# Performance work log

Hardware: AMD Instinct MI355X
Metric: run time of the kernel (lower is better)

Reference implementation:

```python
import jax, jax.numpy as jnp
import numpy as np

HID = 128      # hidden_features
NF = 32        # noise_features
NPL = NF // 4  # noise features per layer
RES = 512      # noise grid resolution
N = 262144     # number of query points


def leaky_relu(x):
    return jax.nn.leaky_relu(x, negative_slope=0.01)


def sample_bilinear(image, coords):
    """image: [M, H, W]; coords: [..., M, 2] -> [..., M]"""
    M, Hn, Wn = image.shape
    x = coords[..., 0] - 0.5
    y = coords[..., 1] - 0.5
    x0f = jnp.floor(x)
    y0f = jnp.floor(y)
    xw = x - x0f
    yw = y - y0f
    x0 = x0f.astype(jnp.int32) % Wn
    x1 = (x0f.astype(jnp.int32) + 1) % Wn
    y0 = y0f.astype(jnp.int32) % Hn
    y1 = (y0f.astype(jnp.int32) + 1) % Hn
    f = jnp.arange(M)  # broadcasts against [..., M] index arrays
    i00 = image[f, y0, x0]
    i01 = image[f, y0, x1]
    i10 = image[f, y1, x0]
    i11 = image[f, y1, x1]
    i0 = i00 + (i01 - i00) * xw
    i1 = i10 + (i11 - i10) * xw
    return i0 + (i1 - i0) * yw


def setup_inputs() -> dict:
    key = jax.random.key(0)
    ks = jax.random.split(key, 12)
    noise = jax.random.normal(ks[0], (NF, RES, RES), dtype=jnp.float32)
    coords = jax.random.normal(ks[1], (N, 2), dtype=jnp.float32)
    # NoiseTransforms param: randn * 0.05 * 2**i per feature
    scale = 0.05 * (2.0 ** np.arange(NF)).astype(np.float32)
    transformations = jax.random.normal(ks[2], (NF, 2, 2), dtype=jnp.float32) * scale[:, None, None]
    input_vec = jnp.ones((HID,), dtype=jnp.float32)
    s_lin = 1.0 / np.sqrt(HID)
    s_noise = 1.0 / np.sqrt(NPL)
    lw = jax.random.uniform(ks[3], (4, HID, HID), jnp.float32, -s_lin, s_lin)
    lb = jax.random.uniform(ks[4], (4, HID), jnp.float32, -s_lin, s_lin)
    lnw = jax.random.uniform(ks[5], (4, HID, NPL), jnp.float32, -s_noise, s_noise)
    tw1 = jax.random.uniform(ks[6], (HID, HID), jnp.float32, -s_lin, s_lin)
    tb1 = jax.random.uniform(ks[7], (HID,), jnp.float32, -s_lin, s_lin)
    tw2 = jax.random.uniform(ks[8], (1, HID), jnp.float32, -s_lin, s_lin)
    tb2 = jax.random.uniform(ks[9], (1,), jnp.float32, -s_lin, s_lin)
    return {"noise": noise, "coords": coords, "transformations": transformations,
            "input_vec": input_vec, "lw": lw, "lb": lb, "lnw": lnw,
            "tw1": tw1, "tb1": tb1, "tw2": tw2, "tb2": tb2}


def reference(noise, coords, transformations, input_vec, lw, lb, lnw, tw1, tb1, tw2, tb2):
    # noise coords: [..., NF, 2]
    noise_coords = jnp.einsum('...n,Mmn->...Mm', coords, transformations)
    noise_values = sample_bilinear(noise, noise_coords)  # [..., NF]
    x = input_vec  # [HID], broadcasts up through layer adds
    for i in range(4):
        nv = noise_values[..., i * NPL:(i + 1) * NPL]
        x = leaky_relu(jnp.einsum('...h,oh->...o', x, lw[i]) + lb[i]
                       + jnp.einsum('...n,on->...o', nv, lnw[i]))
    h = leaky_relu(jnp.einsum('...h,oh->...o', x, tw1) + tb1)
    return jnp.einsum('...h,oh->...o', h, tw2) + tb2  # [..., 1]
```

## Files before the change

kernel.cpp:

```cpp
#include <hip/hip_runtime.h>

typedef _Float16 f16;
typedef f16 f16x4 __attribute__((ext_vector_type(4)));
typedef f16 f16x8 __attribute__((ext_vector_type(8)));
typedef float f32x4 __attribute__((ext_vector_type(4)));

#define RES 512
#define PTS 128
#define XS  138
#define AS  18


__device__ __forceinline__
void pack_w_body(int g, const float* __restrict__ lw, const float* __restrict__ lnw,
                 const float* __restrict__ lb, const float* __restrict__ tw1,
                 const float* __restrict__ tb1, const float* __restrict__ ivec,
                 f16* __restrict__ wf, f16* __restrict__ waugf) {
    if (g < 10240) {
        const int L = g >> 11, r = g & 2047;
        const int lane = r & 63, frag = r >> 6;
        const int q = lane >> 4, l15 = lane & 15;
        const int mt = frag >> 2, c = frag & 3;
        const float* src = ((L < 4) ? (lw + L * 16384) : tw1)
                           + (mt * 16 + l15) * 128 + c * 32 + q * 8;
        f16x8 h;
        #pragma unroll
        for (int j = 0; j < 8; ++j) h[j] = (f16)src[j];
        *(f16x8*)(wf + (size_t)g * 8) = h;
    } else {
        const int ga = g - 10240;
        const int L = ga >> 9, r = ga & 511;
        const int lane = r & 63, mt = r >> 6;
        const int q = lane >> 4, l15 = lane & 15;
        const int row = mt * 16 + l15;
        f16x8 h = {};
        if (q == 0 && L < 4) {
            const float* src = lnw + L * 1024 + row * 8;
            #pragma unroll
            for (int j = 0; j < 8; ++j) h[j] = (f16)src[j];
        }
        if (q == 1) {
            if (L == 0) {
                float s = lb[row];
                const float4* w4 = (const float4*)(lw + row * 128);
                const float4* v4 = (const float4*)ivec;
                #pragma unroll 8
                for (int k = 0; k < 32; ++k) {
                    const float4 w = w4[k], v = v4[k];
                    s += w.x * v.x + w.y * v.y + w.z * v.z + w.w * v.w;
                }
                h[0] = (f16)s;
            } else {
                h[0] = (f16)((L < 4) ? lb[L * 128 + row] : tb1[row]);
            }
        }
        *(f16x8*)(waugf + (size_t)ga * 8) = h;
    }
}

__global__ __launch_bounds__(256)
void pack_all_k(const float* __restrict__ n, f16* __restrict__ q,
                const float* __restrict__ lw,  const float* __restrict__ lnw,
                const float* __restrict__ lb,  const float* __restrict__ tw1,
                const float* __restrict__ tb1, const float* __restrict__ ivec,
                f16* __restrict__ wf, f16* __restrict__ waugf) {
    const int b = blockIdx.x;
    if (b < 8192) {
        const int idx = b * 256 + threadIdx.x;
        const int qx = idx & 255, rest = idx >> 8;
        const int qy = rest & 255, m = rest >> 8;
        const float* src = n + ((size_t)m * 512 + 2 * qy) * 512 + 2 * qx;
        const float2 r0 = *(const float2*)(src);
        const float2 r1 = *(const float2*)(src + 512);
        f16x4 o; o[0]=(f16)r0.x; o[1]=(f16)r0.y; o[2]=(f16)r1.x; o[3]=(f16)r1.y;
        *(f16x4*)(q + (size_t)idx * 4) = o;
    } else {
        pack_w_body((b - 8192) * 256 + threadIdx.x, lw, lnw, lb, tw1, tb1, ivec, wf, waugf);
    }
}

__global__ __launch_bounds__(256)
void pack_w_k(const float* __restrict__ lw,  const float* __restrict__ lnw,
              const float* __restrict__ lb,  const float* __restrict__ tw1,
              const float* __restrict__ tb1, const float* __restrict__ ivec,
              f16* __restrict__ wf, f16* __restrict__ waugf) {
    pack_w_body(blockIdx.x * 256 + threadIdx.x, lw, lnw, lb, tw1, tb1, ivec, wf, waugf);
}

__device__ __forceinline__ float quad_tap(uint2 q, int sy, int sx) {
    unsigned w = sy ? q.y : q.x;
    w >>= (sx << 4);
    union { unsigned short u; f16 h; } cv; cv.u = (unsigned short)w;
    return (float)cv.h;
}

template <bool QUAD>
__global__ __launch_bounds__(256, 8)
void sample_kernel(const void* __restrict__ noise_v,
                   const float* __restrict__ coords,
                   const float* __restrict__ trans,
                   f16* __restrict__ nv_ws, const int Ntot)
{
    __shared__ float T_sh[128];
    const int t = threadIdx.x;
    if (t < 128) T_sh[t] = trans[t];
    __syncthreads();

    const int g = blockIdx.x & 7;
    const int p = (blockIdx.x >> 3) * 256 + t;

    int mk[4];
    if (g < 7) { mk[0] = g; mk[1] = g + 9; mk[2] = g + 17; mk[3] = g + 25; }
    else       { mk[0] = 7; mk[1] = 8;     mk[2] = 16;     mk[3] = 24;     }

    const float2 c2 = *(const float2*)(coords + p * 2);

    float nvr[4];
    {
        #pragma clang fp contract(off)
        const float cx = c2.x;
        const float cy = c2.y;
        #pragma unroll
        for (int k = 0; k < 4; ++k) {
            const int m = mk[k];
            const float T00 = T_sh[m*4+0], T01 = T_sh[m*4+1];
            const float T10 = T_sh[m*4+2], T11 = T_sh[m*4+3];
            const float p0x = T00 * cx;
            const float p0y = T10 * cx;
            const float ncx = __builtin_fmaf(T01, cy, p0x);
            const float ncy = __builtin_fmaf(T11, cy, p0y);
            const float u = ncx - 0.5f;
            const float v = ncy - 0.5f;
            const float xf = floorf(u), yf = floorf(v);
            const float xw = u - xf, yw = v - yf;
            int ix = (xf >= 2147483648.0f || xf < -2147483648.0f) ? (int)(-2147483647 - 1) : (int)xf;
            int iy = (yf >= 2147483648.0f || yf < -2147483648.0f) ? (int)(-2147483647 - 1) : (int)yf;
            const int x0 = ix & (RES - 1);
            const int x1 = (int)(((unsigned)ix + 1u) & (unsigned)(RES - 1));
            const int y0 = iy & (RES - 1);
            const int y1 = (int)(((unsigned)iy + 1u) & (unsigned)(RES - 1));
            float i00, i01, i10, i11;
            if constexpr (QUAD) {
                const f16* pl = (const f16*)noise_v + (size_t)m * (256 * 256 * 4);
                const int qx0 = x0 >> 1, sx0 = x0 & 1;
                const int qx1 = x1 >> 1, sx1 = x1 & 1;
                const int qy0 = y0 >> 1, sy0 = y0 & 1;
                const int qy1 = y1 >> 1, sy1 = y1 & 1;
                const uint2 qa = *(const uint2*)(pl + (qy0 * 256 + qx0) * 4);
                const uint2 qb = *(const uint2*)(pl + (qy0 * 256 + qx1) * 4);
                const uint2 qc = *(const uint2*)(pl + (qy1 * 256 + qx0) * 4);
                const uint2 qd = *(const uint2*)(pl + (qy1 * 256 + qx1) * 4);
                i00 = quad_tap(qa, sy0, sx0);
                i01 = quad_tap(qb, sy0, sx1);
                i10 = quad_tap(qc, sy1, sx0);
                i11 = quad_tap(qd, sy1, sx1);
            } else {
                const float* pl = (const float*)noise_v + (size_t)m * (RES * RES);
                i00 = pl[y0 * RES + x0];
                i01 = pl[y0 * RES + x1];
                i10 = pl[y1 * RES + x0];
                i11 = pl[y1 * RES + x1];
            }
            const float a0 = i00 + (i01 - i00) * xw;
            const float a1 = i10 + (i11 - i10) * xw;
            nvr[k] = a0 + (a1 - a0) * yw;
        }
    }
    #pragma unroll
    for (int k = 0; k < 4; ++k) {
        const int m = mk[k];
        const int slot = (m & 7) * 4 + (m >> 3);
        nv_ws[(size_t)slot * Ntot + p] = (f16)nvr[k];
    }
}

__global__ __launch_bounds__(256, 2)
void mlp_kernel(const f16* __restrict__ nv_ws,
                const f16* __restrict__ wf,
                const f16* __restrict__ waugf,
                const float* __restrict__ tw2,
                const float* __restrict__ tb2,
                float* __restrict__ out, const int Ntot)
{
    __shared__ f16 Wm[16384];
    __shared__ f16 Waug[4096];
    __shared__ f16 xa[PTS * XS];
    __shared__ f16 xaug[PTS * AS];
    __shared__ __align__(16) float tw2_sh[128];

    const int t    = threadIdx.x;
    const int wave = t >> 6;
    const int lane = t & 63;
    const int q    = lane >> 4;
    const int l15  = lane & 15;
    const int pbase = blockIdx.x * PTS;
    const int pw    = wave * 32;
    const int p = t >> 1, h = t & 1;

    if (t < 128) {
        tw2_sh[t] = tw2[t];
        xaug[t * AS + 8] = (f16)1.0f;
        #pragma unroll
        for (int c = 9; c < 16; ++c) xaug[t * AS + c] = (f16)0.0f;
    }
    const float tb2_0 = tb2[0];

    f16x8 nva, nvb;
    {
        const int P = pbase + p;
        #pragma unroll
        for (int j = 0; j < 8; ++j) {
            nva[j] = nv_ws[(size_t)(j * 4 + 2 * h)     * Ntot + P];
            nvb[j] = nv_ws[(size_t)(j * 4 + 2 * h + 1) * Ntot + P];
        }
    }
    if (h == 0) *(f16x8*)&xaug[p * AS] = nva;

    f32x4 acc[2][8];
    #pragma unroll 1
    for (int L = 0; L < 5; ++L) {
        __syncthreads();
        {
            if (L) {
                const f16* wsrc = wf + L * 16384;
                #pragma unroll
                for (int i = 0; i < 8; ++i) {
                    const int idx = t + i * 256;
                    *(f16x8*)&Wm[idx * 8] = *(const f16x8*)&wsrc[idx * 8];
                }
            }
            const f16* asrc = waugf + L * 4096;
            *(f16x8*)&Waug[t * 8]         = *(const f16x8*)&asrc[t * 8];
            *(f16x8*)&Waug[(t + 256) * 8] = *(const f16x8*)&asrc[(t + 256) * 8];
        }
        __syncthreads();

        {
            const f32x4 z4 = {0.f, 0.f, 0.f, 0.f};
            #pragma unroll
            for (int i = 0; i < 2; ++i)
                #pragma unroll
                for (int mt = 0; mt < 8; ++mt) acc[i][mt] = z4;
        }
        if (L) {
            const int pr0 = (pw + l15) * XS, pr1 = (pw + 16 + l15) * XS;
            #pragma unroll
            for (int c = 0; c < 4; ++c) {
                const int kc = c * 32 + q * 8;
                const f16x8 xb0 = *(const f16x8*)&xa[pr0 + kc];
                const f16x8 xb1 = *(const f16x8*)&xa[pr1 + kc];
                #pragma unroll
                for (int mt = 0; mt < 8; ++mt) {
                    const f16x8 aw = *(const f16x8*)&Wm[((mt * 4 + c) * 64 + lane) * 8];
                    acc[0][mt] = __builtin_amdgcn_mfma_f32_16x16x32_f16(aw, xb0, acc[0][mt], 0, 0, 0);
                    acc[1][mt] = __builtin_amdgcn_mfma_f32_16x16x32_f16(aw, xb1, acc[1][mt], 0, 0, 0);
                }
            }
        }
        {
            f16x8 xb0 = {}, xb1 = {};
            if (q < 2) {
                xb0 = *(const f16x8*)&xaug[(pw + l15) * AS + q * 8];
                xb1 = *(const f16x8*)&xaug[(pw + 16 + l15) * AS + q * 8];
            }
            #pragma unroll
            for (int mt = 0; mt < 8; ++mt) {
                const f16x8 aw = *(const f16x8*)&Waug[(mt * 64 + lane) * 8];
                acc[0][mt] = __builtin_amdgcn_mfma_f32_16x16x32_f16(aw, xb0, acc[0][mt], 0, 0, 0);
                acc[1][mt] = __builtin_amdgcn_mfma_f32_16x16x32_f16(aw, xb1, acc[1][mt], 0, 0, 0);
            }
        }

        if (L < 4) {
            #pragma unroll
            for (int i = 0; i < 2; ++i) {
                const int pr = (pw + i * 16 + l15) * XS;
                #pragma unroll
                for (int mt = 0; mt < 8; ++mt) {
                    f16x4 hv;
                    #pragma unroll
                    for (int r = 0; r < 4; ++r) {
                        float v = acc[i][mt][r];
                        v = fmaxf(v, 0.01f * v);
                        hv[r] = (f16)v;
                    }
                    *(f16x4*)&xa[pr + mt * 16 + q * 4] = hv;
                }
            }
            if (L < 3) {
                const int Ln = L + 1;
                if ((Ln >> 1) == h)
                    *(f16x8*)&xaug[p * AS] = (Ln & 1) ? nvb : nva;
            }
        } else {
            #pragma unroll
            for (int i = 0; i < 2; ++i) {
                float s = 0.f;
                #pragma unroll
                for (int mt = 0; mt < 8; ++mt) {
                    const f32x4 w4 = *(const f32x4*)&tw2_sh[mt * 16 + q * 4];
                    #pragma unroll
                    for (int r = 0; r < 4; ++r) {
                        float v = acc[i][mt][r];
                        v = fmaxf(v, 0.01f * v);
                        s += w4[r] * v;
                    }
                }
                s += __shfl_xor(s, 16);
                s += __shfl_xor(s, 32);
                if (q == 0) out[pbase + pw + i * 16 + l15] = s + tb2_0;
            }
        }
    }
}

extern "C" void kernel_launch(void* const* d_in, const int* in_sizes, int n_in,
                              void* d_out, int out_size, void* d_ws, size_t ws_size,
                              hipStream_t stream) {
    const float* noise  = (const float*)d_in[0];
    const float* coords = (const float*)d_in[1];
    const float* trans  = (const float*)d_in[2];
    const float* ivec   = (const float*)d_in[3];
    const float* lw     = (const float*)d_in[4];
    const float* lb     = (const float*)d_in[5];
    const float* lnw    = (const float*)d_in[6];
    const float* tw1    = (const float*)d_in[7];
    const float* tb1    = (const float*)d_in[8];
    const float* tw2    = (const float*)d_in[9];
    const float* tb2    = (const float*)d_in[10];
    float* o            = (float*)d_out;

    const int N = in_sizes[1] / 2;
    f16* nv    = (f16*)d_ws;
    const size_t NV = (size_t)N * 32;
    f16* wfp   = nv + NV;
    f16* waugp = wfp + 5 * 16384;
    f16* qn    = waugp + 5 * 4096;
    const size_t need_full = (NV + 5 * 16384 + 5 * 4096
                              + (size_t)32 * 256 * 256 * 4) * sizeof(f16);

    if (ws_size >= need_full) {
        pack_all_k<<<8192 + 50, 256, 0, stream>>>(noise, qn, lw, lnw, lb, tw1, tb1,
                                                  ivec, wfp, waugp);
        sample_kernel<true><<<(N / 256) * 8, 256, 0, stream>>>(qn, coords, trans, nv, N);
    } else {
        pack_w_k<<<50, 256, 0, stream>>>(lw, lnw, lb, tw1, tb1, ivec, wfp, waugp);
        sample_kernel<false><<<(N / 256) * 8, 256, 0, stream>>>(noise, coords, trans, nv, N);
    }
    mlp_kernel<<<N / PTS, 256, 0, stream>>>(nv, wfp, waugp, tw2, tb2, o, N);
}
```

Measured before the change: 223.8 us.

## Keep MLP weight fragments in registers, split output features across waves

The MLP kernel stops staging each layer's weight matrix in shared memory. Each wave now loads its own 32 output-feature weight fragments straight from global memory into registers and loops over all 128 points of the tile, reading activations from shared memory. This removes the per-layer cooperative weight copy and frees about 40KB of LDS, so launch bounds are raised to allow three blocks per CU. In exchange, every wave reads all activations, each layer needs an extra barrier between computing and writing activations, and the final output needs a cross-wave reduction through shared memory.

```diff
diff --git a/kernel.cpp b/kernel.cpp
--- a/kernel.cpp
+++ b/kernel.cpp
@@ -174,7 +174,7 @@
     }
 }
 
-__global__ __launch_bounds__(256, 2)
+__global__ __launch_bounds__(256, 3)
 void mlp_kernel(const f16* __restrict__ nv_ws,
                 const f16* __restrict__ wf,
                 const f16* __restrict__ waugf,
@@ -182,11 +182,9 @@
                 const float* __restrict__ tb2,
                 float* __restrict__ out, const int Ntot)
 {
-    __shared__ f16 Wm[16384];
-    __shared__ f16 Waug[4096];
     __shared__ f16 xa[PTS * XS];
     __shared__ f16 xaug[PTS * AS];
-    __shared__ __align__(16) float tw2_sh[128];
+    __shared__ float pp[4][PTS];
 
     const int t    = threadIdx.x;
     const int wave = t >> 6;
@@ -194,11 +192,9 @@
     const int q    = lane >> 4;
     const int l15  = lane & 15;
     const int pbase = blockIdx.x * PTS;
-    const int pw    = wave * 32;
     const int p = t >> 1, h = t & 1;
 
     if (t < 128) {
-        tw2_sh[t] = tw2[t];
         xaug[t * AS + 8] = (f16)1.0f;
         #pragma unroll
         for (int c = 9; c < 16; ++c) xaug[t * AS + c] = (f16)0.0f;
@@ -215,76 +211,70 @@
         }
     }
     if (h == 0) *(f16x8*)&xaug[p * AS] = nva;
+    __syncthreads();
 
     f32x4 acc[2][8];
     #pragma unroll 1
     for (int L = 0; L < 5; ++L) {
-        __syncthreads();
-        {
-            if (L) {
-                const f16* wsrc = wf + L * 16384;
-                #pragma unroll
-                for (int i = 0; i < 8; ++i) {
-                    const int idx = t + i * 256;
-                    *(f16x8*)&Wm[idx * 8] = *(const f16x8*)&wsrc[idx * 8];
-                }
-            }
-            const f16* asrc = waugf + L * 4096;
-            *(f16x8*)&Waug[t * 8]         = *(const f16x8*)&asrc[t * 8];
-            *(f16x8*)&Waug[(t + 256) * 8] = *(const f16x8*)&asrc[(t + 256) * 8];
-        }
-        __syncthreads();
+        f16x8 awm[2][4], awa[2];
+        if (L) {
+            #pragma unroll
+            for (int mtl = 0; mtl < 2; ++mtl)
+                #pragma unroll
+                for (int c = 0; c < 4; ++c)
+                    awm[mtl][c] = *(const f16x8*)
+                        &wf[(size_t)((L * 32 + (wave * 2 + mtl) * 4 + c) * 64 + lane) * 8];
+        }
+        #pragma unroll
+        for (int mtl = 0; mtl < 2; ++mtl)
+            awa[mtl] = *(const f16x8*)
+                &waugf[(size_t)((L * 8 + wave * 2 + mtl) * 64 + lane) * 8];
 
         {
             const f32x4 z4 = {0.f, 0.f, 0.f, 0.f};
             #pragma unroll
-            for (int i = 0; i < 2; ++i)
-                #pragma unroll
-                for (int mt = 0; mt < 8; ++mt) acc[i][mt] = z4;
+            for (int mtl = 0; mtl < 2; ++mtl)
+                #pragma unroll
+                for (int pt = 0; pt < 8; ++pt) acc[mtl][pt] = z4;
         }
         if (L) {
-            const int pr0 = (pw + l15) * XS, pr1 = (pw + 16 + l15) * XS;
             #pragma unroll
             for (int c = 0; c < 4; ++c) {
                 const int kc = c * 32 + q * 8;
-                const f16x8 xb0 = *(const f16x8*)&xa[pr0 + kc];
-                const f16x8 xb1 = *(const f16x8*)&xa[pr1 + kc];
-                #pragma unroll
-                for (int mt = 0; mt < 8; ++mt) {
-                    const f16x8 aw = *(const f16x8*)&Wm[((mt * 4 + c) * 64 + lane) * 8];
-                    acc[0][mt] = __builtin_amdgcn_mfma_f32_16x16x32_f16(aw, xb0, acc[0][mt], 0, 0, 0);
-                    acc[1][mt] = __builtin_amdgcn_mfma_f32_16x16x32_f16(aw, xb1, acc[1][mt], 0, 0, 0);
+                #pragma unroll
+                for (int pt = 0; pt < 8; ++pt) {
+                    const f16x8 xb = *(const f16x8*)&xa[(pt * 16 + l15) * XS + kc];
+                    acc[0][pt] = __builtin_amdgcn_mfma_f32_16x16x32_f16(awm[0][c], xb, acc[0][pt], 0, 0, 0);
+                    acc[1][pt] = __builtin_amdgcn_mfma_f32_16x16x32_f16(awm[1][c], xb, acc[1][pt], 0, 0, 0);
                 }
             }
         }
         {
-            f16x8 xb0 = {}, xb1 = {};
-            if (q < 2) {
-                xb0 = *(const f16x8*)&xaug[(pw + l15) * AS + q * 8];
-                xb1 = *(const f16x8*)&xaug[(pw + 16 + l15) * AS + q * 8];
-            }
-            #pragma unroll
-            for (int mt = 0; mt < 8; ++mt) {
-                const f16x8 aw = *(const f16x8*)&Waug[(mt * 64 + lane) * 8];
-                acc[0][mt] = __builtin_amdgcn_mfma_f32_16x16x32_f16(aw, xb0, acc[0][mt], 0, 0, 0);
-                acc[1][mt] = __builtin_amdgcn_mfma_f32_16x16x32_f16(aw, xb1, acc[1][mt], 0, 0, 0);
-            }
-        }
+            #pragma unroll
+            for (int pt = 0; pt < 8; ++pt) {
+                f16x8 xb = {};
+                if (q < 2) xb = *(const f16x8*)&xaug[(pt * 16 + l15) * AS + q * 8];
+                acc[0][pt] = __builtin_amdgcn_mfma_f32_16x16x32_f16(awa[0], xb, acc[0][pt], 0, 0, 0);
+                acc[1][pt] = __builtin_amdgcn_mfma_f32_16x16x32_f16(awa[1], xb, acc[1][pt], 0, 0, 0);
+            }
+        }
+
+        __syncthreads();
 
         if (L < 4) {
             #pragma unroll
-            for (int i = 0; i < 2; ++i) {
-                const int pr = (pw + i * 16 + l15) * XS;
-                #pragma unroll
-                for (int mt = 0; mt < 8; ++mt) {
+            for (int mtl = 0; mtl < 2; ++mtl) {
+                const int fc = wave * 32 + mtl * 16 + q * 4;
+                #pragma unroll
+                for (int pt = 0; pt < 8; ++pt) {
                     f16x4 hv;
                     #pragma unroll
                     for (int r = 0; r < 4; ++r) {
-                        float v = acc[i][mt][r];
+                        float v = acc[mtl][pt][r];
                         v = fmaxf(v, 0.01f * v);
                         hv[r] = (f16)v;
                     }
-                    *(f16x4*)&xa[pr + mt * 16 + q * 4] = hv;
+                    *(f16x4*)&xa[(pt * 16 + l15) * XS + fc] = hv;
                 }
             }
             if (L < 3) {
@@ -292,24 +282,28 @@
                 if ((Ln >> 1) == h)
                     *(f16x8*)&xaug[p * AS] = (Ln & 1) ? nvb : nva;
             }
+            __syncthreads();
         } else {
-            #pragma unroll
-            for (int i = 0; i < 2; ++i) {
+            const f32x4 w40 = *(const f32x4*)&tw2[wave * 32 + q * 4];
+            const f32x4 w41 = *(const f32x4*)&tw2[wave * 32 + 16 + q * 4];
+            #pragma unroll
+            for (int pt = 0; pt < 8; ++pt) {
                 float s = 0.f;
                 #pragma unroll
-                for (int mt = 0; mt < 8; ++mt) {
-                    const f32x4 w4 = *(const f32x4*)&tw2_sh[mt * 16 + q * 4];
-                    #pragma unroll
-                    for (int r = 0; r < 4; ++r) {
-                        float v = acc[i][mt][r];
-                        v = fmaxf(v, 0.01f * v);
-                        s += w4[r] * v;
-                    }
+                for (int r = 0; r < 4; ++r) {
+                    float v0 = acc[0][pt][r];
+                    v0 = fmaxf(v0, 0.01f * v0);
+                    float v1 = acc[1][pt][r];
+                    v1 = fmaxf(v1, 0.01f * v1);
+                    s += w40[r] * v0 + w41[r] * v1;
                 }
                 s += __shfl_xor(s, 16);
                 s += __shfl_xor(s, 32);
-                if (q == 0) out[pbase + pw + i * 16 + l15] = s + tb2_0;
-            }
+                if (q == 0) pp[wave][pt * 16 + l15] = s;
+            }
+            __syncthreads();
+            if (t < 128)
+                out[pbase + t] = pp[0][t] + pp[1][t] + pp[2][t] + pp[3][t] + tb2_0;
         }
     }
 }
```

Result: slower. 282.9 us (+26.4%).
